# Performance work log

Hardware: AMD Instinct MI355X
Metric: run time of the kernel (lower is better)

## Reference

```python
import jax, jax.numpy as jnp
import numpy as np

EPS = 1e-08

def setup_inputs() -> dict:
    key = jax.random.key(0)
    k1, k2 = jax.random.split(key)
    h = jax.random.normal(k1, (4096, 512), dtype=jnp.float32)   # [B, D]
    A = jax.random.normal(k2, (32768, 512), dtype=jnp.float32)  # [K, D]
    return {"h": h, "A": A}

def _l2_normalize(x, eps=EPS):
    # matches torch F.normalize(p=2): x / max(||x||, eps)
    n = jnp.sqrt(jnp.sum(x * x, axis=-1, keepdims=True))
    return x / jnp.maximum(n, eps)

def reference(h, A):
    # cosine metric: normalize both, matmul, argmax over K
    h_n = _l2_normalize(h)                      # [B, D]
    A_n = _l2_normalize(A)                      # [K, D]
    scores = jnp.einsum('bd,kd->bk', h_n, A_n)  # [B, K]
    idx = jnp.argmax(scores, axis=1, keepdims=True)  # [B, 1] int
    return idx
```

## Files before the change

kernel.cpp:

```cpp
#include <hip/hip_runtime.h>
#include <stdint.h>


#define DIM 512
#define B_ROWS 4096
#define K_ROWS 32768
#define BT 128
#define KT 128
#define NKT (K_ROWS / KT)
#define KSLOTS 32
#define NCHUNK 4
#define QSCALE (127.0f / 0.26f)

typedef __attribute__((ext_vector_type(4))) float fx4;
typedef __attribute__((ext_vector_type(4))) int int4v;
typedef unsigned long long u64;

__device__ __forceinline__ uint32_t ford(float s) {
    uint32_t u = __float_as_uint(s);
    return u ^ ((uint32_t)((int32_t)u >> 31) | 0x80000000u);
}
__device__ __forceinline__ u64 umax64(u64 a, u64 b) { return a > b ? a : b; }
__device__ __forceinline__ u64 umin64(u64 a, u64 b) { return a < b ? a : b; }
__device__ __forceinline__ uint32_t umax32(uint32_t a, uint32_t b) { return a > b ? a : b; }
__device__ __forceinline__ uint32_t umin32(uint32_t a, uint32_t b) { return a < b ? a : b; }

__device__ __forceinline__ int q8(float x, float qs) {
    int v = __float2int_rn(x * qs);
    return v < -127 ? -127 : (v > 127 ? 127 : v);
}

__global__ __launch_bounds__(256) void prep_kernel(const float* __restrict__ A,
                                                   const float* __restrict__ h,
                                                   char* __restrict__ a8,
                                                   char* __restrict__ h8,
                                                   float* __restrict__ rn) {
    const int lane = threadIdx.x & 63, wid = threadIdx.x >> 6;
    const bool isA = blockIdx.x < 8192;
    const int row = (isA ? blockIdx.x : blockIdx.x - 8192) * 4 + wid;
    const float* src = (isA ? A : h) + (size_t)row * DIM;
    char* dst = (isA ? a8 : h8) + (size_t)row * DIM;

    const fx4* p = (const fx4*)src;
    fx4 a = p[lane * 2], b = p[lane * 2 + 1];
    float ss = a[0]*a[0] + a[1]*a[1] + a[2]*a[2] + a[3]*a[3]
             + b[0]*b[0] + b[1]*b[1] + b[2]*b[2] + b[3]*b[3];
    #pragma unroll
    for (int off = 32; off > 0; off >>= 1) ss += __shfl_xor(ss, off, 64);
    float r = 1.0f / fmaxf(sqrtf(ss), 1e-8f);
    if (isA && lane == 0) rn[row] = r;

    float qs = r * QSCALE;
    int v0 = q8(a[0], qs), v1 = q8(a[1], qs), v2 = q8(a[2], qs), v3 = q8(a[3], qs);
    int v4 = q8(b[0], qs), v5 = q8(b[1], qs), v6 = q8(b[2], qs), v7 = q8(b[3], qs);
    uint32_t lo = (uint32_t)(v0 & 255) | ((uint32_t)(v1 & 255) << 8)
                | ((uint32_t)(v2 & 255) << 16) | ((uint32_t)(v3 & 255) << 24);
    uint32_t hi = (uint32_t)(v4 & 255) | ((uint32_t)(v5 & 255) << 8)
                | ((uint32_t)(v6 & 255) << 16) | ((uint32_t)(v7 & 255) << 24);
    *reinterpret_cast<uint2*>(dst + lane * 8) = make_uint2(lo, hi);
}

typedef __attribute__((address_space(3))) uint32_t lds_u32;
typedef __attribute__((address_space(1))) const uint32_t g_u32;

__global__ __launch_bounds__(256, 3) void score_kernel(
    const char* __restrict__ h8, const char* __restrict__ a8,
    u64* __restrict__ cand)
{
    __shared__ __attribute__((aligned(16))) char smem[33792];
    char* hf = smem;
    char* af = smem + 16384;

    const int t = threadIdx.x, lane = t & 63, wid = t >> 6;
    const int wm = wid >> 1, wn = wid & 1;
    const int lr = lane & 15, q = lane >> 4;
    const int btile = blockIdx.x >> 5, kslot = blockIdx.x & 31;
    const int b0 = btile * BT;

    const int srow = lane >> 3;
    const int scol = (lane & 7) ^ srow;
    const int s7 = lr & 7;
    const int sw0 = (q ^ s7) * 16;
    const int sw1 = ((4 + q) ^ s7) * 16;

    const char* hsrc = h8 + (size_t)b0 * DIM;

    uint32_t v1[16], v2[16];
    #pragma unroll
    for (int s = 0; s < 16; s++) { v1[s] = 0u; v2[s] = 0u; }

    int it = 0;
    #pragma unroll 1
    for (int kt = kslot; kt < NKT; kt += KSLOTS, it++) {
        const int k0 = kt * KT;
        const char* asrc = a8 + (size_t)k0 * DIM;

        int4v acc[4][4];
        #pragma unroll
        for (int mi = 0; mi < 4; mi++)
            #pragma unroll
            for (int ni = 0; ni < 4; ni++)
                acc[mi][ni] = (int4v){0, 0, 0, 0};

        #pragma unroll 1
        for (int dc = 0; dc < NCHUNK; dc++) {
            __syncthreads();
            #pragma unroll
            for (int i = 0; i < 4; i++) {
                int issue = wid * 4 + i;
                size_t roff = (size_t)(issue * 8 + srow) * DIM + dc * 128 + scol * 16;
                __builtin_amdgcn_global_load_lds((g_u32*)(hsrc + roff),
                    (lds_u32*)(hf + issue * 1024), 16, 0, 0);
                __builtin_amdgcn_global_load_lds((g_u32*)(asrc + roff),
                    (lds_u32*)(af + issue * 1024), 16, 0, 0);
            }
            __syncthreads();

            int4v af0[4], af1[4];
            #pragma unroll
            for (int ni = 0; ni < 4; ni++) {
                const char* base = af + (wn * 64 + ni * 16 + lr) * 128;
                af0[ni] = *reinterpret_cast<const int4v*>(base + sw0);
                af1[ni] = *reinterpret_cast<const int4v*>(base + sw1);
            }
            #pragma unroll
            for (int mi = 0; mi < 4; mi++) {
                const char* base = hf + (wm * 64 + mi * 16 + lr) * 128;
                int4v h0 = *reinterpret_cast<const int4v*>(base + sw0);
                int4v h1 = *reinterpret_cast<const int4v*>(base + sw1);
                #pragma unroll
                for (int ni = 0; ni < 4; ni++) {
                    acc[mi][ni] = __builtin_amdgcn_mfma_i32_16x16x64_i8(h0, af0[ni], acc[mi][ni], 0, 0, 0);
                    acc[mi][ni] = __builtin_amdgcn_mfma_i32_16x16x64_i8(h1, af1[ni], acc[mi][ni], 0, 0, 0);
                }
            }
        }

        const uint32_t metabase = (uint32_t)(it << 2);
        #pragma unroll
        for (int mi = 0; mi < 4; mi++)
            #pragma unroll
            for (int ni = 0; ni < 4; ni++) {
                const uint32_t meta = metabase | (uint32_t)ni;
                #pragma unroll
                for (int r = 0; r < 4; r++) {
                    uint32_t ord = (uint32_t)acc[mi][ni][r] ^ 0x80000000u;
                    uint32_t pk = (ord & 0xFFFFFFC0u) | meta;
                    int s = mi * 4 + r;
                    uint32_t lo = umin32(v1[s], pk);
                    v1[s] = umax32(v1[s], pk);
                    v2[s] = umax32(v2[s], lo);
                }
            }
    }

    uint32_t* cl = (uint32_t*)smem;
    u64 g1 = 0, g2 = 0, g3 = 0;
    for (int pass = 0; pass < 2; pass++) {
        __syncthreads();
        #pragma unroll
        for (int s = 0; s < 16; s++) {
            int mi = s >> 2, r = s & 3;
            int row_local = wm * 64 + mi * 16 + q * 4 + r;
            cl[row_local * 33 + wn * 16 + lr] = pass ? v2[s] : v1[s];
        }
        __syncthreads();
        if (t < BT) {
            #pragma unroll 4
            for (int j = 0; j < 32; j++) {
                uint32_t pv = cl[t * 33 + j];
                uint32_t meta = pv & 63u;
                int k = (kslot + (int)(meta >> 2) * KSLOTS) * KT
                      + (j >> 4) * 64 + (int)(meta & 3u) * 16 + (j & 15);
                u64 e = ((u64)(pv & 0xFFFFFFC0u) << 32) | (u64)(~(uint32_t)k);
                u64 t1 = umax64(g1, e), t2 = umin64(g1, e);
                g3 = umax64(g3, umin64(g2, t2));
                g2 = umax64(g2, t2);
                g1 = t1;
            }
        }
    }
    if (t < BT) {
        size_t base = ((size_t)(b0 + t) * KSLOTS + kslot) * 3;
        cand[base] = g1;
        cand[base + 1] = g2;
        cand[base + 2] = g3;
    }
}

__global__ __launch_bounds__(256) void refine_kernel(
    const float* __restrict__ h, const float* __restrict__ A,
    const float* __restrict__ rn, const u64* __restrict__ cand,
    int* __restrict__ out)
{
    const int t = threadIdx.x, lane = t & 63, wid = t >> 6;
    const int row = blockIdx.x * 4 + wid;
    const u64* cr = cand + (size_t)row * (KSLOTS * 3);
    u64 x0 = cr[lane];
    u64 x1 = (lane < KSLOTS * 3 - 64) ? cr[64 + lane] : 0ULL;

    u64 sel[8];
    #pragma unroll
    for (int j = 0; j < 8; j++) {
        u64 v = umax64(x0, x1);
        #pragma unroll
        for (int m = 32; m >= 1; m >>= 1) v = umax64(v, __shfl_xor(v, m, 64));
        sel[j] = v;
        if (x0 == v) x0 = 0;
        else if (x1 == v) x1 = 0;
    }

    const fx4* hp = reinterpret_cast<const fx4*>(h + (size_t)row * DIM);
    fx4 h0 = hp[lane * 2], h1 = hp[lane * 2 + 1];

    u64 best = 0;
    #pragma unroll
    for (int j = 0; j < 8; j++) {
        uint32_t kg = ~(uint32_t)sel[j];
        const fx4* ap = reinterpret_cast<const fx4*>(A + (size_t)kg * DIM);
        fx4 a0 = ap[lane * 2], a1 = ap[lane * 2 + 1];
        float s = h0[0]*a0[0] + h0[1]*a0[1] + h0[2]*a0[2] + h0[3]*a0[3]
                + h1[0]*a1[0] + h1[1]*a1[1] + h1[2]*a1[2] + h1[3]*a1[3];
        #pragma unroll
        for (int m = 32; m >= 1; m >>= 1) s += __shfl_xor(s, m, 64);
        s *= rn[kg];
        u64 pk = ((u64)ford(s) << 32) | (u64)(~kg);
        best = umax64(best, pk);
    }
    if (lane == 0) out[row] = (int)(~(uint32_t)best);
}

extern "C" void kernel_launch(void* const* d_in, const int* in_sizes, int n_in,
                              void* d_out, int out_size, void* d_ws, size_t ws_size,
                              hipStream_t stream) {
    const float* h = (const float*)d_in[0];
    const float* A = (const float*)d_in[1];
    int* out = (int*)d_out;

    char* w = (char*)d_ws;
    char* a8 = w;
    char* h8 = w + (size_t)K_ROWS * DIM;
    float* rn = (float*)(w + (size_t)(K_ROWS + B_ROWS) * DIM);
    u64* cand = (u64*)(w + (size_t)(K_ROWS + B_ROWS) * DIM
                         + (size_t)K_ROWS * sizeof(float));

    prep_kernel<<<8192 + 1024, 256, 0, stream>>>(A, h, a8, h8, rn);
    score_kernel<<<32 * KSLOTS, 256, 0, stream>>>(h8, a8, cand);
    refine_kernel<<<B_ROWS / 4, 256, 0, stream>>>(h, A, rn, cand, out);
}
```

Measured before the change: 206.8 us.

## Keep h tile resident in LDS and stream pre-swizzled A fragments into registers

```diff
diff --git a/kernel.cpp b/kernel.cpp
--- a/kernel.cpp
+++ b/kernel.cpp
@@ -8,7 +8,8 @@
 #define BT 128
 #define KT 128
 #define NKT (K_ROWS / KT)
-#define KSLOTS 32
+#define KSLOTS 16
+#define NKTPB (NKT / KSLOTS)
 #define NCHUNK 4
 #define QSCALE (127.0f / 0.26f)
 
@@ -32,14 +33,13 @@
 
 __global__ __launch_bounds__(256) void prep_kernel(const float* __restrict__ A,
                                                    const float* __restrict__ h,
-                                                   char* __restrict__ a8,
+                                                   char* __restrict__ a8s,
                                                    char* __restrict__ h8,
                                                    float* __restrict__ rn) {
     const int lane = threadIdx.x & 63, wid = threadIdx.x >> 6;
     const bool isA = blockIdx.x < 8192;
     const int row = (isA ? blockIdx.x : blockIdx.x - 8192) * 4 + wid;
     const float* src = (isA ? A : h) + (size_t)row * DIM;
-    char* dst = (isA ? a8 : h8) + (size_t)row * DIM;
 
     const fx4* p = (const fx4*)src;
     fx4 a = p[lane * 2], b = p[lane * 2 + 1];
@@ -57,24 +57,32 @@
                 | ((uint32_t)(v2 & 255) << 16) | ((uint32_t)(v3 & 255) << 24);
     uint32_t hi = (uint32_t)(v4 & 255) | ((uint32_t)(v5 & 255) << 8)
                 | ((uint32_t)(v6 & 255) << 16) | ((uint32_t)(v7 & 255) << 24);
-    *reinterpret_cast<uint2*>(dst + lane * 8) = make_uint2(lo, hi);
+
+    if (!isA) {
+        *reinterpret_cast<uint2*>(h8 + (size_t)row * DIM + lane * 8) = make_uint2(lo, hi);
+    } else {
+        int kt = row >> 7, wnr = (row >> 6) & 1, ni = (row >> 4) & 3, m = row & 15;
+        int dc = lane >> 4, rem = lane & 15;
+        int ks = rem >> 3, q = (rem >> 1) & 3, j0 = (lane & 1) * 8;
+        size_t off = (size_t)kt * 65536 + (size_t)dc * 16384 + wnr * 8192
+                   + ni * 2048 + ks * 1024 + q * 256 + m * 16 + j0;
+        *reinterpret_cast<uint2*>(a8s + off) = make_uint2(lo, hi);
+    }
 }
 
 typedef __attribute__((address_space(3))) uint32_t lds_u32;
 typedef __attribute__((address_space(1))) const uint32_t g_u32;
 
-__global__ __launch_bounds__(256, 3) void score_kernel(
-    const char* __restrict__ h8, const char* __restrict__ a8,
+__global__ __launch_bounds__(256, 2) void score_kernel(
+    const char* __restrict__ h8, const char* __restrict__ a8s,
     u64* __restrict__ cand)
 {
-    __shared__ __attribute__((aligned(16))) char smem[33792];
-    char* hf = smem;
-    char* af = smem + 16384;
+    __shared__ __attribute__((aligned(16))) char smem[65536];
 
     const int t = threadIdx.x, lane = t & 63, wid = t >> 6;
     const int wm = wid >> 1, wn = wid & 1;
     const int lr = lane & 15, q = lane >> 4;
-    const int btile = blockIdx.x >> 5, kslot = blockIdx.x & 31;
+    const int btile = blockIdx.x & 31, kslot = blockIdx.x >> 5;
     const int b0 = btile * BT;
 
     const int srow = lane >> 3;
@@ -83,18 +91,36 @@
     const int sw0 = (q ^ s7) * 16;
     const int sw1 = ((4 + q) ^ s7) * 16;
 
-    const char* hsrc = h8 + (size_t)b0 * DIM;
+    {
+        const char* hsrc = h8 + (size_t)b0 * DIM;
+        #pragma unroll
+        for (int i = 0; i < 16; i++) {
+            int issue = wid * 16 + i;
+            int dc = issue >> 4, rb = issue & 15;
+            const char* g = hsrc + (size_t)(rb * 8 + srow) * DIM + dc * 128 + scol * 16;
+            __builtin_amdgcn_global_load_lds((g_u32*)g, (lds_u32*)(smem + issue * 1024), 16, 0, 0);
+        }
+    }
+    __syncthreads();
 
     uint32_t v1[16], v2[16];
     #pragma unroll
     for (int s = 0; s < 16; s++) { v1[s] = 0u; v2[s] = 0u; }
 
-    int it = 0;
+    const char* abase = a8s + (size_t)lane * 16 + wn * 8192;
+    #define A_ADDR(cc) (abase + (size_t)(kslot + ((cc) >> 2) * KSLOTS) * 65536 \
+                              + (size_t)((cc) & 3) * 16384)
+
+    int4v Ab[2][8];
+    {
+        const char* nb = A_ADDR(0);
+        #pragma unroll
+        for (int u = 0; u < 8; u++)
+            Ab[0][u] = *reinterpret_cast<const int4v*>(nb + (u >> 1) * 2048 + (u & 1) * 1024);
+    }
+
     #pragma unroll 1
-    for (int kt = kslot; kt < NKT; kt += KSLOTS, it++) {
-        const int k0 = kt * KT;
-        const char* asrc = a8 + (size_t)k0 * DIM;
-
+    for (int kt_i = 0; kt_i < NKTPB; kt_i++) {
         int4v acc[4][4];
         #pragma unroll
         for (int mi = 0; mi < 4; mi++)
@@ -102,41 +128,33 @@
             for (int ni = 0; ni < 4; ni++)
                 acc[mi][ni] = (int4v){0, 0, 0, 0};
 
-        #pragma unroll 1
+        #pragma unroll
         for (int dc = 0; dc < NCHUNK; dc++) {
-            __syncthreads();
-            #pragma unroll
-            for (int i = 0; i < 4; i++) {
-                int issue = wid * 4 + i;
-                size_t roff = (size_t)(issue * 8 + srow) * DIM + dc * 128 + scol * 16;
-                __builtin_amdgcn_global_load_lds((g_u32*)(hsrc + roff),
-                    (lds_u32*)(hf + issue * 1024), 16, 0, 0);
-                __builtin_amdgcn_global_load_lds((g_u32*)(asrc + roff),
-                    (lds_u32*)(af + issue * 1024), 16, 0, 0);
-            }
-            __syncthreads();
-
-            int4v af0[4], af1[4];
-            #pragma unroll
-            for (int ni = 0; ni < 4; ni++) {
-                const char* base = af + (wn * 64 + ni * 16 + lr) * 128;
-                af0[ni] = *reinterpret_cast<const int4v*>(base + sw0);
-                af1[ni] = *reinterpret_cast<const int4v*>(base + sw1);
-            }
+            const int cc = kt_i * 4 + dc;
+            const int ncc = (cc < NKTPB * 4 - 1) ? cc + 1 : cc;
+            const char* nb = A_ADDR(ncc);
+            #pragma unroll
+            for (int u = 0; u < 8; u++)
+                Ab[(dc + 1) & 1][u] =
+                    *reinterpret_cast<const int4v*>(nb + (u >> 1) * 2048 + (u & 1) * 1024);
+
+            const char* hc = smem + dc * 16384;
             #pragma unroll
             for (int mi = 0; mi < 4; mi++) {
-                const char* base = hf + (wm * 64 + mi * 16 + lr) * 128;
-                int4v h0 = *reinterpret_cast<const int4v*>(base + sw0);
-                int4v h1 = *reinterpret_cast<const int4v*>(base + sw1);
+                const char* hb = hc + (wm * 64 + mi * 16 + lr) * 128;
+                int4v h0 = *reinterpret_cast<const int4v*>(hb + sw0);
+                int4v h1 = *reinterpret_cast<const int4v*>(hb + sw1);
                 #pragma unroll
                 for (int ni = 0; ni < 4; ni++) {
-                    acc[mi][ni] = __builtin_amdgcn_mfma_i32_16x16x64_i8(h0, af0[ni], acc[mi][ni], 0, 0, 0);
-                    acc[mi][ni] = __builtin_amdgcn_mfma_i32_16x16x64_i8(h1, af1[ni], acc[mi][ni], 0, 0, 0);
+                    acc[mi][ni] = __builtin_amdgcn_mfma_i32_16x16x64_i8(
+                        h0, Ab[dc & 1][ni * 2], acc[mi][ni], 0, 0, 0);
+                    acc[mi][ni] = __builtin_amdgcn_mfma_i32_16x16x64_i8(
+                        h1, Ab[dc & 1][ni * 2 + 1], acc[mi][ni], 0, 0, 0);
                 }
             }
         }
 
-        const uint32_t metabase = (uint32_t)(it << 2);
+        const uint32_t metabase = (uint32_t)(kt_i << 2);
         #pragma unroll
         for (int mi = 0; mi < 4; mi++)
             #pragma unroll
@@ -196,18 +214,16 @@
     const int t = threadIdx.x, lane = t & 63, wid = t >> 6;
     const int row = blockIdx.x * 4 + wid;
     const u64* cr = cand + (size_t)row * (KSLOTS * 3);
-    u64 x0 = cr[lane];
-    u64 x1 = (lane < KSLOTS * 3 - 64) ? cr[64 + lane] : 0ULL;
+    u64 x = (lane < KSLOTS * 3) ? cr[lane] : 0ULL;
 
     u64 sel[8];
     #pragma unroll
     for (int j = 0; j < 8; j++) {
-        u64 v = umax64(x0, x1);
+        u64 v = x;
         #pragma unroll
         for (int m = 32; m >= 1; m >>= 1) v = umax64(v, __shfl_xor(v, m, 64));
         sel[j] = v;
-        if (x0 == v) x0 = 0;
-        else if (x1 == v) x1 = 0;
+        if (x == v) x = 0;
     }
 
     const fx4* hp = reinterpret_cast<const fx4*>(h + (size_t)row * DIM);
@@ -238,13 +254,13 @@
     int* out = (int*)d_out;
 
     char* w = (char*)d_ws;
-    char* a8 = w;
+    char* a8s = w;
     char* h8 = w + (size_t)K_ROWS * DIM;
     float* rn = (float*)(w + (size_t)(K_ROWS + B_ROWS) * DIM);
     u64* cand = (u64*)(w + (size_t)(K_ROWS + B_ROWS) * DIM
                          + (size_t)K_ROWS * sizeof(float));
 
-    prep_kernel<<<8192 + 1024, 256, 0, stream>>>(A, h, a8, h8, rn);
-    score_kernel<<<32 * KSLOTS, 256, 0, stream>>>(h8, a8, cand);
+    prep_kernel<<<8192 + 1024, 256, 0, stream>>>(A, h, a8s, h8, rn);
+    score_kernel<<<32 * KSLOTS, 256, 0, stream>>>(h8, a8s, cand);
     refine_kernel<<<B_ROWS / 4, 256, 0, stream>>>(h, A, rn, cand, out);
 }
```

New measurement: 222.4 us. 1.08x slower.
